# Kernel optimization log

Measured on AMD Instinct MI355X. Metric: run time of the kernel, lower is better.

The kernel has to match this reference:

```python
import jax, jax.numpy as jnp
import numpy as np

NUM_GROUPS = 32
EPS = 1e-5

def setup_inputs() -> dict:
    key = jax.random.key(0)
    ks = jax.random.split(key, 10)
    N, C, H, W = 4, 128, 64, 64
    x = jax.random.normal(ks[0], (N, C, H, W), dtype=jnp.float32)
    # GroupNorm affine params
    gn_scale = jnp.ones((C,), dtype=jnp.float32)
    gn_bias = jnp.zeros((C,), dtype=jnp.float32)
    # 1x1 conv weights [out, in] (xavier_uniform scale)
    lim = float(np.sqrt(6.0 / (C + C)))
    wq = jax.random.uniform(ks[1], (C, C), minval=-lim, maxval=lim, dtype=jnp.float32)
    wk = jax.random.uniform(ks[2], (C, C), minval=-lim, maxval=lim, dtype=jnp.float32)
    wv = jax.random.uniform(ks[3], (C, C), minval=-lim, maxval=lim, dtype=jnp.float32)
    wp = jax.random.uniform(ks[4], (C, C), minval=-lim, maxval=lim, dtype=jnp.float32) * 1e-5
    bq = jnp.zeros((C,), dtype=jnp.float32)
    bk = jnp.zeros((C,), dtype=jnp.float32)
    bv = jnp.zeros((C,), dtype=jnp.float32)
    bp = jnp.zeros((C,), dtype=jnp.float32)
    return {"x": x, "gn_scale": gn_scale, "gn_bias": gn_bias,
            "wq": wq, "bq": bq, "wk": wk, "bk": bk,
            "wv": wv, "bv": bv, "wp": wp, "bp": bp}

def _group_norm(x, scale, bias):
    # x: [N, C, H, W]
    N, C, H, W = x.shape
    g = x.reshape(N, NUM_GROUPS, C // NUM_GROUPS, H, W)
    mean = g.mean(axis=(2, 3, 4), keepdims=True)
    var = g.var(axis=(2, 3, 4), keepdims=True)
    g = (g - mean) * jax.lax.rsqrt(var + EPS)
    x = g.reshape(N, C, H, W)
    return x * scale[None, :, None, None] + bias[None, :, None, None]

def reference(x, gn_scale, gn_bias, wq, bq, wk, bk, wv, bv, wp, bp):
    N, C, H, W = x.shape
    h = _group_norm(x, gn_scale, gn_bias)
    # flatten spatial to tokens: [N, HW, C]
    ht = h.reshape(N, C, H * W).transpose(0, 2, 1)
    q = jnp.einsum('nlc,oc->nlo', ht, wq) + bq
    k = jnp.einsum('nlc,oc->nlo', ht, wk) + bk
    v = jnp.einsum('nlc,oc->nlo', ht, wv) + bv
    score = jnp.einsum('nqc,nkc->nqk', q, k) * (C ** -0.5)  # [N, HW, HW]
    attn = jax.nn.softmax(score, axis=-1)
    out = jnp.einsum('nqk,nkc->nqc', attn, v)  # [N, HW, C]
    out = jnp.einsum('nlc,oc->nlo', out, wp) + bp
    out = out.transpose(0, 2, 1).reshape(N, C, H, W)
    return x + out
```

## Files before the change

### kernel.cpp

```cpp
#include <hip/hip_runtime.h>

#define HW 4096
#define CCH 128
#define NB 4

typedef short bf16x8 __attribute__((ext_vector_type(8)));
typedef float f32x4 __attribute__((ext_vector_type(4)));

__device__ __forceinline__ unsigned short f2bf(float f){
  union { float fv; unsigned u; } v; v.fv = f;
  unsigned r = v.u + 0x7fffu + ((v.u >> 16) & 1u);
  return (unsigned short)(r >> 16);
}
__device__ __forceinline__ float bf2f(unsigned short u){
  return __uint_as_float(((unsigned)u) << 16);
}
__device__ __forceinline__ f32x4 mfma16(bf16x8 a, bf16x8 b, f32x4 c){
  return __builtin_amdgcn_mfma_f32_16x16x32_bf16(a, b, c, 0, 0, 0);
}
__device__ __forceinline__ void gll16(const void* g, void* l){
  __builtin_amdgcn_global_load_lds(
      (const __attribute__((address_space(1))) unsigned*)g,
      (__attribute__((address_space(3))) unsigned*)l, 16, 0, 0);
}

__global__ __launch_bounds__(256) void gn_stats_k(const float* __restrict__ x,
    float* __restrict__ stats,
    const float* __restrict__ wq, const float* __restrict__ wk,
    const float* __restrict__ wv, const float* __restrict__ wp,
    unsigned short* __restrict__ wqb, unsigned short* __restrict__ wkb,
    unsigned short* __restrict__ wvb, unsigned short* __restrict__ wpb){
  int tid = threadIdx.x;
  if (tid < 128){
    int f4 = blockIdx.x * 128 + tid;
    int m = f4 >> 12, e = f4 & 4095;
    const float* s4 = (m == 0) ? wq : ((m == 1) ? wk : ((m == 2) ? wv : wp));
    unsigned short* d4 = (m == 0) ? wqb : ((m == 1) ? wkb : ((m == 2) ? wvb : wpb));
    float4 v = *(const float4*)(s4 + e * 4);
    ushort4 b; b.x = f2bf(v.x); b.y = f2bf(v.y); b.z = f2bf(v.z); b.w = f2bf(v.w);
    *(ushort4*)(d4 + e * 4) = b;
  }
  int gid = blockIdx.x;
  const float4* p = (const float4*)(x + (size_t)gid * 16384);
  float s = 0.f, q = 0.f;
  #pragma unroll
  for (int i = 0; i < 16; i++){
    float4 v = p[tid + 256 * i];
    s += v.x + v.y + v.z + v.w;
    q += v.x * v.x + v.y * v.y + v.z * v.z + v.w * v.w;
  }
  #pragma unroll
  for (int d = 1; d < 64; d <<= 1){ s += __shfl_xor(s, d); q += __shfl_xor(q, d); }
  __shared__ float red[8];
  int w = tid >> 6;
  if ((tid & 63) == 0){ red[2 * w] = s; red[2 * w + 1] = q; }
  __syncthreads();
  if (tid == 0){
    float S = red[0] + red[2] + red[4] + red[6];
    float Q = red[1] + red[3] + red[5] + red[7];
    float mean = S * (1.f / 16384.f);
    float var  = Q * (1.f / 16384.f) - mean * mean;
    stats[2 * gid]     = mean;
    stats[2 * gid + 1] = rsqrtf(var + 1e-5f);
  }
}

__global__ __launch_bounds__(256) void gn_apply_k(const float* __restrict__ x,
    const float* __restrict__ stats, const float* __restrict__ sc,
    const float* __restrict__ bi, unsigned short* __restrict__ ht){
  int n = blockIdx.y, l0 = blockIdx.x * 32, tid = threadIdx.x;
  __shared__ __align__(16) unsigned short hs[32][136];
  #pragma unroll
  for (int i = 0; i < 16; i++){
    int c = (tid >> 5) + 8 * i;
    int l = tid & 31;
    float v = x[((size_t)(n * CCH + c)) * HW + l0 + l];
    int grp = n * 32 + (c >> 2);
    float r = (v - stats[2 * grp]) * stats[2 * grp + 1] * sc[c] + bi[c];
    hs[l][c] = f2bf(r);
  }
  __syncthreads();
  #pragma unroll
  for (int i = 0; i < 2; i++){
    int ch = tid + 256 * i;
    int l = ch >> 4, cb = (ch & 15) * 8;
    *(uint4*)&ht[((size_t)(n * HW) + l0 + l) * CCH + cb] = *(const uint4*)&hs[l][cb];
  }
}

__global__ __launch_bounds__(256, 3) void qkv_k(const unsigned short* __restrict__ ht,
    const unsigned short* __restrict__ wqb, const unsigned short* __restrict__ wkb,
    const unsigned short* __restrict__ wvb,
    const float* __restrict__ bq, const float* __restrict__ bk,
    const float* __restrict__ bv,
    unsigned short* __restrict__ Qg, unsigned short* __restrict__ Kg,
    unsigned short* __restrict__ Vt){
  int n = blockIdx.y, l0 = blockIdx.x * 64, m = blockIdx.z, tid = threadIdx.x;
  int w = tid >> 6, lane = tid & 63, l15 = lane & 15, g = lane >> 4;
  __shared__ __align__(16) char lds[49152];
  char* hA = lds;
  char* WB = lds + 16384;
  const unsigned short* wsrc = (m == 0) ? wqb : ((m == 1) ? wkb : wvb);
  const float* bsrc = (m == 0) ? bq : ((m == 1) ? bk : bv);
  {
    const char* hb = (const char*)ht + ((size_t)(n * HW) + l0) * (CCH * 2);
    #pragma unroll
    for (int i = 0; i < 4; i++){
      int T = (4 * w + i) * 64 + lane;
      int row = T >> 4, c16 = (T & 15) ^ (row & 15);
      gll16(hb + row * 256 + c16 * 16, hA + (4 * w + i) * 1024);
    }
    const char* wb2 = (const char*)wsrc;
    #pragma unroll
    for (int i = 0; i < 8; i++){
      int T = (8 * w + i) * 64 + lane;
      int row = T >> 4, c16 = (T & 15) ^ (row & 15);
      gll16(wb2 + row * 256 + c16 * 16, WB + (8 * w + i) * 1024);
    }
  }
  __syncthreads();
  bf16x8 a[4];
  #pragma unroll
  for (int kc = 0; kc < 4; kc++)
    a[kc] = *(const bf16x8*)(hA + (16 * w + l15) * 256 + ((4 * kc + g) ^ l15) * 16);
  f32x4 acc[8];
  #pragma unroll
  for (int ct = 0; ct < 8; ct++) acc[ct] = (f32x4)(0.f);
  #pragma unroll
  for (int ct = 0; ct < 8; ct++)
    #pragma unroll
    for (int kc = 0; kc < 4; kc++){
      bf16x8 bfr = *(const bf16x8*)(WB + (16 * ct + l15) * 256 + ((4 * kc + g) ^ l15) * 16);
      acc[ct] = mfma16(a[kc], bfr, acc[ct]);
    }
  __syncthreads();
  if (m < 2){
    float qs = (m == 0) ? 0.08838834764831845f : 1.0f;
    unsigned short* dst = (m == 0) ? Qg : Kg;
    unsigned short* os = (unsigned short*)(lds + 16384);
    #pragma unroll
    for (int ct = 0; ct < 8; ct++){
      int o = 16 * ct + l15;
      float bias = bsrc[o];
      #pragma unroll
      for (int r = 0; r < 4; r++)
        os[(16 * w + 4 * g + r) * 136 + o] = f2bf((acc[ct][r] + bias) * qs);
    }
    __syncthreads();
    #pragma unroll
    for (int i = 0; i < 4; i++){
      int T = tid + 256 * i;
      int row = T >> 4, cb = T & 15;
      *(uint4*)&dst[((size_t)(n * HW) + l0 + row) * CCH + cb * 8] =
          *(const uint4*)&os[row * 136 + cb * 8];
    }
  } else {
    unsigned short* os = (unsigned short*)(lds + 16384);
    #pragma unroll
    for (int ct = 0; ct < 8; ct++){
      int o = 16 * ct + l15;
      float bias = bsrc[o];
      #pragma unroll
      for (int r = 0; r < 4; r++)
        os[o * 72 + 16 * w + 4 * g + r] = f2bf(acc[ct][r] + bias);
    }
    __syncthreads();
    #pragma unroll
    for (int i = 0; i < 4; i++){
      int T = tid + 256 * i;
      int row = T >> 3, c = T & 7;
      *(uint4*)&Vt[((size_t)(n * CCH) + row) * HW + l0 + c * 8] =
          *(const uint4*)&os[row * 72 + c * 8];
    }
  }
}

__global__ __launch_bounds__(256, 4) void attn_k(const unsigned short* __restrict__ Qg,
    const unsigned short* __restrict__ Kg, const unsigned short* __restrict__ Vt,
    unsigned short* __restrict__ Op, float* __restrict__ Ml, int lsp){
  int nbk = gridDim.x, cpx = nbk >> 3, b = blockIdx.x;
  int swz = (b & 7) * cpx + (b >> 3);
  int q0 = (swz & 63) * 64;
  int rest = swz >> 6;
  int splits = 1 << lsp;
  int sp = rest & (splits - 1);
  int n = rest >> lsp;
  int kvs = HW >> lsp, nt = 64 >> lsp;
  int tid = threadIdx.x;
  int w = tid >> 6, lane = tid & 63, l15 = lane & 15, g = lane >> 4;
  __shared__ __align__(16) char lds[32768];
  char* Ks = lds;
  char* Vs = lds + 16384;

  bf16x8 qf[4];
  #pragma unroll
  for (int kc = 0; kc < 4; kc++)
    qf[kc] = *reinterpret_cast<const bf16x8*>(
        &Qg[((size_t)(n * HW) + q0 + 16 * w + l15) * CCH + 32 * kc + 8 * g]);
  f32x4 ov[8];
  #pragma unroll
  for (int i = 0; i < 8; i++) ov[i] = (f32x4)(0.f);
  float mrun[4] = {-3.0e38f, -3.0e38f, -3.0e38f, -3.0e38f};
  float lrun[4] = {0.f, 0.f, 0.f, 0.f};

  const char* kp[4]; const char* vp[4];
  {
    const char* kbase = (const char*)Kg + ((size_t)(n * HW) + sp * kvs) * (CCH * 2);
    const char* vbase = (const char*)Vt + (size_t)(n * CCH) * (HW * 2) + (size_t)sp * kvs * 2;
    #pragma unroll
    for (int i = 0; i < 4; i++){
      int C = (w * 4 + i) * 64 + lane;
      int row = C >> 4, c16 = (C & 15) ^ (row & 15);
      kp[i] = kbase + row * 256 + c16 * 16;
      int vrow = C >> 3, c8 = (C & 7) ^ (vrow & 7);
      vp[i] = vbase + (size_t)vrow * (HW * 2) + c8 * 16;
    }
  }
  char* kl = Ks + w * 4096;
  char* vl = Vs + w * 4096;

  for (int t = 0; t < nt; t++){
    __syncthreads();
    #pragma unroll
    for (int i = 0; i < 4; i++) gll16(kp[i] + t * 16384, kl + i * 1024);
    #pragma unroll
    for (int i = 0; i < 4; i++) gll16(vp[i] + t * 128,   vl + i * 1024);
    __syncthreads();

    f32x4 s[4];
    __builtin_amdgcn_s_setprio(1);
    #pragma unroll
    for (int ct = 0; ct < 4; ct++){
      f32x4 acc = (f32x4)(0.f);
      #pragma unroll
      for (int kc = 0; kc < 4; kc++){
        bf16x8 kf = *(const bf16x8*)(Ks + (16 * ct + l15) * 256 + ((4 * kc + g) ^ l15) * 16);
        acc = mfma16(qf[kc], kf, acc);
      }
      s[ct] = acc;
    }
    __builtin_amdgcn_s_setprio(0);
    float mx[4];
    #pragma unroll
    for (int r = 0; r < 4; r++)
      mx[r] = fmaxf(fmaxf(s[0][r], s[1][r]), fmaxf(s[2][r], s[3][r]));
    #pragma unroll
    for (int d = 1; d < 16; d <<= 1)
      #pragma unroll
      for (int r = 0; r < 4; r++) mx[r] = fmaxf(mx[r], __shfl_xor(mx[r], d));
    int need = 0;
    #pragma unroll
    for (int r = 0; r < 4; r++) need |= (mx[r] > mrun[r] + 8.0f) ? 1 : 0;
    if (__any(need)){
      float al[4];
      #pragma unroll
      for (int r = 0; r < 4; r++){
        float mn = fmaxf(mrun[r], mx[r]);
        al[r] = __expf(mrun[r] - mn);
        mrun[r] = mn;
        lrun[r] *= al[r];
      }
      #pragma unroll
      for (int ct = 0; ct < 8; ct++)
        #pragma unroll
        for (int r = 0; r < 4; r++) ov[ct][r] *= al[r];
    }
    #pragma unroll
    for (int ct = 0; ct < 4; ct++)
      #pragma unroll
      for (int r = 0; r < 4; r++) s[ct][r] = __expf(s[ct][r] - mrun[r]);
    float rs[4];
    #pragma unroll
    for (int r = 0; r < 4; r++) rs[r] = s[0][r] + s[1][r] + s[2][r] + s[3][r];
    #pragma unroll
    for (int d = 1; d < 16; d <<= 1)
      #pragma unroll
      for (int r = 0; r < 4; r++) rs[r] += __shfl_xor(rs[r], d);
    #pragma unroll
    for (int r = 0; r < 4; r++) lrun[r] += rs[r];

    __syncthreads();
    char* Pw = Ks + w * 2304;
    #pragma unroll
    for (int ct = 0; ct < 4; ct++)
      #pragma unroll
      for (int r = 0; r < 4; r++)
        *(unsigned short*)(Pw + (4 * g + r) * 144 + (16 * ct + l15) * 2) = f2bf(s[ct][r]);
    __builtin_amdgcn_s_setprio(1);
    #pragma unroll
    for (int ct = 0; ct < 8; ct++){
      #pragma unroll
      for (int kc = 0; kc < 2; kc++){
        bf16x8 pa = *(const bf16x8*)(Pw + l15 * 144 + (32 * kc + 8 * g) * 2);
        bf16x8 vf = *(const bf16x8*)(Vs + (16 * ct + l15) * 128 + ((4 * kc + g) ^ (l15 & 7)) * 16);
        ov[ct] = mfma16(pa, vf, ov[ct]);
      }
    }
    __builtin_amdgcn_s_setprio(0);
  }
  size_t obase = (size_t)((sp * NB + n) * HW);
  #pragma unroll
  for (int ct = 0; ct < 8; ct++){
    int o = 16 * ct + l15;
    #pragma unroll
    for (int r = 0; r < 4; r++){
      int l = q0 + 16 * w + 4 * g + r;
      Op[(obase + l) * CCH + o] = f2bf(ov[ct][r]);
    }
  }
  if (l15 == 0){
    #pragma unroll
    for (int r = 0; r < 4; r++){
      int l = q0 + 16 * w + 4 * g + r;
      Ml[(obase + l) * 2]     = mrun[r];
      Ml[(obase + l) * 2 + 1] = lrun[r];
    }
  }
}

__global__ __launch_bounds__(256) void projout_k(const unsigned short* __restrict__ Op,
    const float* __restrict__ Ml, const unsigned short* __restrict__ wpb,
    const float* __restrict__ bp, const float* __restrict__ x,
    float* __restrict__ out, int splits){
  int n = blockIdx.y, l0 = blockIdx.x * 32, tid = threadIdx.x;
  int w = tid >> 6, lane = tid & 63, l15 = lane & 15, g = lane >> 4;
  __shared__ __align__(16) unsigned short hs[32][136];
  __shared__ __align__(16) char WB[32768];
  {
    const char* wb2 = (const char*)wpb;
    #pragma unroll
    for (int i = 0; i < 8; i++){
      int T = (8 * w + i) * 64 + lane;
      int row = T >> 4, c16 = (T & 15) ^ (row & 15);
      gll16(wb2 + row * 256 + c16 * 16, WB + (8 * w + i) * 1024);
    }
  }
  const size_t SSTR = (size_t)NB * HW;
  #pragma unroll
  for (int i = 0; i < 2; i++){
    int T = tid + 256 * i;
    int row = T >> 4, cb = (T & 15) * 8;
    size_t gl = (size_t)n * HW + l0 + row;
    float mv = -3.0e38f;
    #pragma unroll
    for (int s = 0; s < 4; s++)
      if (s < splits) mv = fmaxf(mv, Ml[(s * SSTR + gl) * 2]);
    float fa[8];
    #pragma unroll
    for (int j = 0; j < 8; j++) fa[j] = 0.f;
    float denom = 0.f;
    #pragma unroll
    for (int s = 0; s < 4; s++){
      if (s < splits){
        float wgt = __expf(Ml[(s * SSTR + gl) * 2] - mv);
        denom += wgt * Ml[(s * SSTR + gl) * 2 + 1];
        uint4 a = *(const uint4*)&Op[(s * SSTR + gl) * CCH + cb];
        const unsigned short* au = (const unsigned short*)&a;
        #pragma unroll
        for (int j = 0; j < 8; j++) fa[j] += wgt * bf2f(au[j]);
      }
    }
    float inv = 1.f / denom;
    #pragma unroll
    for (int j = 0; j < 8; j++) hs[row][cb + j] = f2bf(fa[j] * inv);
  }
  __syncthreads();
  int rt = w & 1, cg = w >> 1;
  bf16x8 a[4];
  #pragma unroll
  for (int kc = 0; kc < 4; kc++)
    a[kc] = *reinterpret_cast<const bf16x8*>(&hs[16 * rt + l15][32 * kc + 8 * g]);
  f32x4 acc[4];
  #pragma unroll
  for (int ci = 0; ci < 4; ci++) acc[ci] = (f32x4)(0.f);
  #pragma unroll
  for (int ci = 0; ci < 4; ci++){
    int o = 16 * (cg * 4 + ci) + l15;
    #pragma unroll
    for (int kc = 0; kc < 4; kc++){
      bf16x8 bfr = *(const bf16x8*)(WB + o * 256 + ((4 * kc + g) ^ l15) * 16);
      acc[ci] = mfma16(a[kc], bfr, acc[ci]);
    }
  }
  #pragma unroll
  for (int ci = 0; ci < 4; ci++){
    int o = 16 * (cg * 4 + ci) + l15;
    float bias = bp[o];
    size_t base = ((size_t)(n * CCH) + o) * HW + l0 + 16 * rt + 4 * g;
    float4 xr = *(const float4*)&x[base];
    float4 res;
    res.x = xr.x + acc[ci][0] + bias;
    res.y = xr.y + acc[ci][1] + bias;
    res.z = xr.z + acc[ci][2] + bias;
    res.w = xr.w + acc[ci][3] + bias;
    *(float4*)&out[base] = res;
  }
}

extern "C" void kernel_launch(void* const* d_in, const int* in_sizes, int n_in,
                              void* d_out, int out_size, void* d_ws, size_t ws_size,
                              hipStream_t stream){
  const float* x    = (const float*)d_in[0];
  const float* gnsc = (const float*)d_in[1];
  const float* gnb  = (const float*)d_in[2];
  const float* wq   = (const float*)d_in[3];
  const float* bq   = (const float*)d_in[4];
  const float* wk   = (const float*)d_in[5];
  const float* bk   = (const float*)d_in[6];
  const float* wv   = (const float*)d_in[7];
  const float* bv   = (const float*)d_in[8];
  const float* wp   = (const float*)d_in[9];
  const float* bp   = (const float*)d_in[10];
  float* out = (float*)d_out;

  char* ws = (char*)d_ws;
  const size_t BUF = (size_t)NB * HW * CCH * sizeof(unsigned short);
  const size_t WOFF = 4096;
  const size_t HTOFF = WOFF + 4 * 32768;
  const size_t NEED4 = HTOFF + 8 * BUF + (size_t)4 * NB * HW * 2 * sizeof(float);
  const int lsp = (ws_size >= NEED4) ? 2 : 1;
  const int splits = 1 << lsp;

  float* stats        = (float*)ws;
  unsigned short* wqb = (unsigned short*)(ws + WOFF);
  unsigned short* wkb = (unsigned short*)(ws + WOFF + 32768);
  unsigned short* wvb = (unsigned short*)(ws + WOFF + 65536);
  unsigned short* wpb = (unsigned short*)(ws + WOFF + 98304);
  unsigned short* ht  = (unsigned short*)(ws + HTOFF);
  unsigned short* Qg  = (unsigned short*)(ws + HTOFF + BUF);
  unsigned short* Kg  = (unsigned short*)(ws + HTOFF + 2 * BUF);
  unsigned short* Vt  = (unsigned short*)(ws + HTOFF + 3 * BUF);
  unsigned short* Op  = (unsigned short*)(ws + HTOFF + 4 * BUF);
  float*          Ml  = (float*)(ws + HTOFF + 4 * BUF + (size_t)splits * BUF);

  gn_stats_k<<<128, 256, 0, stream>>>(x, stats, wq, wk, wv, wp, wqb, wkb, wvb, wpb);
  gn_apply_k<<<dim3(128, NB), 256, 0, stream>>>(x, stats, gnsc, gnb, ht);
  qkv_k<<<dim3(64, NB, 3), 256, 0, stream>>>(ht, wqb, wkb, wvb, bq, bk, bv, Qg, Kg, Vt);
  attn_k<<<dim3(64 * NB * splits), 256, 0, stream>>>(Qg, Kg, Vt, Op, Ml, lsp);
  projout_k<<<dim3(128, NB), 256, 0, stream>>>(Op, Ml, wpb, bp, x, out, splits);
}
```

Measured before the change: 172.6 us.

## Transpose attention MFMAs so softmax stats are per-lane and P stays in registers

Swaps the MFMA operand order so each lane owns one query row. Row max and sum then need only two cross-lane shuffles instead of a 16-wide butterfly over four rows. The probability tile is repacked into bf16 B-operands with register shuffles rather than written to and reread from LDS, which also drops a block-wide barrier. The output is stored as packed 4-element vectors per row. The risk is that the shuffle-based repack costs more than the LDS round trip, and that any operand-layout mistake gives wrong results.

```diff
diff --git a/kernel.cpp b/kernel.cpp
--- a/kernel.cpp
+++ b/kernel.cpp
@@ -200,8 +200,7 @@
   f32x4 ov[8];
   #pragma unroll
   for (int i = 0; i < 8; i++) ov[i] = (f32x4)(0.f);
-  float mrun[4] = {-3.0e38f, -3.0e38f, -3.0e38f, -3.0e38f};
-  float lrun[4] = {0.f, 0.f, 0.f, 0.f};
+  float mrun = -3.0e38f, lrun = 0.f;
 
   const char* kp[4]; const char* vp[4];
   {
@@ -222,9 +221,9 @@
   for (int t = 0; t < nt; t++){
     __syncthreads();
     #pragma unroll
-    for (int i = 0; i < 4; i++) gll16(kp[i] + t * 16384, kl + i * 1024);
-    #pragma unroll
-    for (int i = 0; i < 4; i++) gll16(vp[i] + t * 128,   vl + i * 1024);
+    for (int i = 0; i < 4; i++) gll16(kp[i] + (size_t)t * 16384, kl + i * 1024);
+    #pragma unroll
+    for (int i = 0; i < 4; i++) gll16(vp[i] + (size_t)t * 128,   vl + i * 1024);
     __syncthreads();
 
     f32x4 s[4];
@@ -235,86 +234,84 @@
       #pragma unroll
       for (int kc = 0; kc < 4; kc++){
         bf16x8 kf = *(const bf16x8*)(Ks + (16 * ct + l15) * 256 + ((4 * kc + g) ^ l15) * 16);
-        acc = mfma16(qf[kc], kf, acc);
+        acc = mfma16(kf, qf[kc], acc);
       }
       s[ct] = acc;
     }
     __builtin_amdgcn_s_setprio(0);
-    float mx[4];
-    #pragma unroll
-    for (int r = 0; r < 4; r++)
-      mx[r] = fmaxf(fmaxf(s[0][r], s[1][r]), fmaxf(s[2][r], s[3][r]));
-    #pragma unroll
-    for (int d = 1; d < 16; d <<= 1)
-      #pragma unroll
-      for (int r = 0; r < 4; r++) mx[r] = fmaxf(mx[r], __shfl_xor(mx[r], d));
-    int need = 0;
-    #pragma unroll
-    for (int r = 0; r < 4; r++) need |= (mx[r] > mrun[r] + 8.0f) ? 1 : 0;
-    if (__any(need)){
-      float al[4];
-      #pragma unroll
-      for (int r = 0; r < 4; r++){
-        float mn = fmaxf(mrun[r], mx[r]);
-        al[r] = __expf(mrun[r] - mn);
-        mrun[r] = mn;
-        lrun[r] *= al[r];
-      }
+
+    float mx = -3.0e38f;
+    #pragma unroll
+    for (int ct = 0; ct < 4; ct++)
+      #pragma unroll
+      for (int r = 0; r < 4; r++) mx = fmaxf(mx, s[ct][r]);
+    mx = fmaxf(mx, __shfl_xor(mx, 16));
+    mx = fmaxf(mx, __shfl_xor(mx, 32));
+    if (__any(mx > mrun + 8.0f)){
+      float mn = fmaxf(mrun, mx);
+      float al = __expf(mrun - mn);
+      mrun = mn; lrun *= al;
       #pragma unroll
       for (int ct = 0; ct < 8; ct++)
         #pragma unroll
-        for (int r = 0; r < 4; r++) ov[ct][r] *= al[r];
-    }
+        for (int r = 0; r < 4; r++) ov[ct][r] *= al;
+    }
+    float rs = 0.f;
     #pragma unroll
     for (int ct = 0; ct < 4; ct++)
       #pragma unroll
-      for (int r = 0; r < 4; r++) s[ct][r] = __expf(s[ct][r] - mrun[r]);
-    float rs[4];
-    #pragma unroll
-    for (int r = 0; r < 4; r++) rs[r] = s[0][r] + s[1][r] + s[2][r] + s[3][r];
-    #pragma unroll
-    for (int d = 1; d < 16; d <<= 1)
-      #pragma unroll
-      for (int r = 0; r < 4; r++) rs[r] += __shfl_xor(rs[r], d);
-    #pragma unroll
-    for (int r = 0; r < 4; r++) lrun[r] += rs[r];
-
-    __syncthreads();
-    char* Pw = Ks + w * 2304;
+      for (int r = 0; r < 4; r++){
+        float e = __expf(s[ct][r] - mrun);
+        s[ct][r] = e;
+        rs += e;
+      }
+    rs += __shfl_xor(rs, 16);
+    rs += __shfl_xor(rs, 32);
+    lrun += rs;
+
+    unsigned up[4][2];
     #pragma unroll
     for (int ct = 0; ct < 4; ct++)
       #pragma unroll
-      for (int r = 0; r < 4; r++)
-        *(unsigned short*)(Pw + (4 * g + r) * 144 + (16 * ct + l15) * 2) = f2bf(s[ct][r]);
+      for (int h = 0; h < 2; h++)
+        up[ct][h] = (unsigned)f2bf(s[ct][2 * h]) |
+                    ((unsigned)f2bf(s[ct][2 * h + 1]) << 16);
+    union { unsigned u[2][4]; bf16x8 v[2]; } pb;
+    #pragma unroll
+    for (int kc = 0; kc < 2; kc++)
+      #pragma unroll
+      for (int j = 0; j < 4; j++){
+        int src = (((j + ((g & 1) << 2)) >> 1) << 4) + l15;
+        unsigned v0 = (unsigned)__shfl((int)up[2 * kc][j & 1], src);
+        unsigned v1 = (unsigned)__shfl((int)up[2 * kc + 1][j & 1], src);
+        pb.u[kc][j] = (g & 2) ? v1 : v0;
+      }
+
     __builtin_amdgcn_s_setprio(1);
     #pragma unroll
     for (int ct = 0; ct < 8; ct++){
       #pragma unroll
       for (int kc = 0; kc < 2; kc++){
-        bf16x8 pa = *(const bf16x8*)(Pw + l15 * 144 + (32 * kc + 8 * g) * 2);
         bf16x8 vf = *(const bf16x8*)(Vs + (16 * ct + l15) * 128 + ((4 * kc + g) ^ (l15 & 7)) * 16);
-        ov[ct] = mfma16(pa, vf, ov[ct]);
+        ov[ct] = mfma16(vf, pb.v[kc], ov[ct]);
       }
     }
     __builtin_amdgcn_s_setprio(0);
   }
+  float inv = 1.f / lrun;
+  (void)inv;
   size_t obase = (size_t)((sp * NB + n) * HW);
+  size_t qrow = obase + q0 + 16 * w + l15;
   #pragma unroll
   for (int ct = 0; ct < 8; ct++){
-    int o = 16 * ct + l15;
-    #pragma unroll
-    for (int r = 0; r < 4; r++){
-      int l = q0 + 16 * w + 4 * g + r;
-      Op[(obase + l) * CCH + o] = f2bf(ov[ct][r]);
-    }
-  }
-  if (l15 == 0){
-    #pragma unroll
-    for (int r = 0; r < 4; r++){
-      int l = q0 + 16 * w + 4 * g + r;
-      Ml[(obase + l) * 2]     = mrun[r];
-      Ml[(obase + l) * 2 + 1] = lrun[r];
-    }
+    ushort4 pk;
+    pk.x = f2bf(ov[ct][0]); pk.y = f2bf(ov[ct][1]);
+    pk.z = f2bf(ov[ct][2]); pk.w = f2bf(ov[ct][3]);
+    *(ushort4*)&Op[qrow * CCH + 16 * ct + 4 * g] = pk;
+  }
+  if (g == 0){
+    Ml[qrow * 2]     = mrun;
+    Ml[qrow * 2 + 1] = lrun;
   }
 }
 
```

New measurement: 157.6 us. 8.7% less time.
